# Performance work log

Hardware: AMD Instinct MI355X
Metric: run time of the kernel (lower is better)

## Reference

```python
import jax, jax.numpy as jnp
import numpy as np

CONF_THRES = 0.25
IOU_THRES = 0.45
MAX_ANCHORS = 50
PRE_NMS_TOPK = 2048   # candidate cap, standard fused-NMS trick to bound the IoU matrix
NEG = -1.0e9
NUM_CLASSES = 80
IMG = 640.0


def setup_inputs() -> dict:
    key = jax.random.key(0)
    k1, k2, k3, k4 = jax.random.split(key, 4)
    B, N = 16, 25200
    # realistic xyxy boxes inside a 640x640 image
    cxcy = jax.random.uniform(k1, (B, N, 2), minval=0.0, maxval=IMG)
    wh = jax.random.uniform(k2, (B, N, 2), minval=4.0, maxval=64.0)
    x1y1 = jnp.clip(cxcy - 0.5 * wh, 0.0, IMG)
    x2y2 = jnp.clip(cxcy + 0.5 * wh, 0.0, IMG)
    conf = jax.random.uniform(k3, (B, N, 1))
    cls = jax.random.randint(k4, (B, N, 1), 0, NUM_CLASSES).astype(jnp.float32)
    x = jnp.concatenate([x1y1, x2y2, conf, cls], axis=-1)  # [B, N, 6]
    return {"x": x}


def _box_iou_matrix(boxes):
    # boxes: [K, 4] xyxy -> [K, K] pairwise IoU
    x1, y1, x2, y2 = boxes[:, 0], boxes[:, 1], boxes[:, 2], boxes[:, 3]
    area = jnp.maximum(x2 - x1, 0.0) * jnp.maximum(y2 - y1, 0.0)  # [K]
    iw = jnp.maximum(jnp.minimum(x2[:, None], x2[None, :]) - jnp.maximum(x1[:, None], x1[None, :]), 0.0)
    ih = jnp.maximum(jnp.minimum(y2[:, None], y2[None, :]) - jnp.maximum(y1[:, None], y1[None, :]), 0.0)
    inter = iw * ih
    union = area[:, None] + area[None, :] - inter
    return inter / jnp.maximum(union, 1e-9)


def _nms_single(bx):
    # bx: [N, 6] -> [MAX_ANCHORS, 6], rows padded with -1 (keep_shape semantics)
    scores = bx[:, 4]
    s = jnp.where(scores > CONF_THRES, scores, NEG)  # confidence filter
    top_s, top_i = jax.lax.top_k(s, PRE_NMS_TOPK)     # sort descending by score
    cand = jnp.take(bx, top_i, axis=0)                # [K, 6]
    cvalid = top_s > 0.5 * NEG                        # passed conf filter

    iou = _box_iou_matrix(cand[:, :4])                # [K, K]
    idxs = jnp.arange(PRE_NMS_TOPK)
    # box i may only suppress lower-scored boxes j > i
    suppr_rows = (iou >= IOU_THRES) & (idxs[None, :] > idxs[:, None])

    def step(suppressed, i):
        keep_i = cvalid[i] & jnp.logical_not(suppressed[i])
        suppressed = suppressed | (keep_i & suppr_rows[i])
        return suppressed, keep_i

    _, keep = jax.lax.scan(step, jnp.zeros(PRE_NMS_TOPK, dtype=bool), idxs)

    final_s = jnp.where(keep, cand[:, 4], NEG)
    sel_s, sel_i = jax.lax.top_k(final_s, MAX_ANCHORS)  # top-50 kept boxes by conf
    rows = jnp.take(cand, sel_i, axis=0)                # [50, 6]
    return jnp.where((sel_s > 0.5 * NEG)[:, None], rows, -1.0)


def reference(x):
    # x: [B, N, 6] -> [B, MAX_ANCHORS, 6]
    return jax.vmap(_nms_single)(x)
```

## Files before the change

### kernel.cpp

```cpp
#include <hip/hip_runtime.h>

#define BATCH   16
#define NANCH   25200
#define TPB     1024
#define NWAVES  (TPB / 64)
#define MAXK    50
#define PRETOPK 2048
#define CONF_T  0.25f
#define IOU_T   0.45f
#define NEGV    -1000000000.0f
#define T0      0.9905f
#define CAP     320

__global__ __launch_bounds__(TPB, 1) void nms_kernel(const float* __restrict__ x,
                                                     float* __restrict__ out) {
    __shared__ float s_scores[NANCH];
    __shared__ unsigned long long s_keys[CAP];
    __shared__ float s_srows[CAP][8];
    __shared__ float s_kx1[MAXK], s_ky1[MAXK], s_kx2[MAXK], s_ky2[MAXK], s_ka[MAXK];
    __shared__ float s_wval[NWAVES];
    __shared__ int   s_widx[NWAVES];
    __shared__ int   s_cnt, s_nk, s_best;

    const int b    = blockIdx.x;
    const int tid  = threadIdx.x;
    const int lane = tid & 63;
    const int wave = tid >> 6;

    const float* __restrict__ xb = x + (size_t)b * NANCH * 6;
    float* __restrict__ ob       = out + (size_t)b * MAXK * 6;

    if (tid < CAP) s_keys[tid] = 0ULL;
    if (tid == 0) { s_cnt = 0; s_nk = 0; }
    __syncthreads();

    {
        int i = tid;
        for (int c = 0; c < 3; ++c) {
            float v[8];
            #pragma unroll
            for (int k = 0; k < 8; ++k) v[k] = xb[(size_t)(i + k * TPB) * 6 + 4];
            #pragma unroll
            for (int k = 0; k < 8; ++k) {
                const int idx = i + k * TPB;
                s_scores[idx] = (v[k] > CONF_T) ? v[k] : NEGV;
                if (v[k] > T0) {
                    int slot = atomicAdd(&s_cnt, 1);
                    if (slot < CAP)
                        s_keys[slot] =
                            ((unsigned long long)__float_as_uint(v[k]) << 32) |
                            ((unsigned long long)(65535 - idx) << 16) |
                            (unsigned long long)slot;
                }
            }
            i += 8 * TPB;
        }
        if (i < NANCH) {
            float s = xb[(size_t)i * 6 + 4];
            s_scores[i] = (s > CONF_T) ? s : NEGV;
            if (s > T0) {
                int slot = atomicAdd(&s_cnt, 1);
                if (slot < CAP)
                    s_keys[slot] =
                        ((unsigned long long)__float_as_uint(s) << 32) |
                        ((unsigned long long)(65535 - i) << 16) |
                        (unsigned long long)slot;
            }
        }
    }
    __syncthreads();

    const int cnt   = s_cnt;
    const bool fast = cnt <= CAP;

    if (fast) {
        if (tid < CAP) {
            const unsigned long long mykey = s_keys[tid];
            float2 r0, r1, r2;
            const bool real = tid < cnt;
            if (real) {
                int myi = 65535 - (int)((mykey >> 16) & 0xFFFFULL);
                const float2* rp = (const float2*)(xb + (size_t)myi * 6);
                r0 = rp[0]; r1 = rp[1]; r2 = rp[2];
            }
            int r = 0;
            #pragma unroll 4
            for (int j = 0; j < CAP; ++j) r += (s_keys[j] > mykey) ? 1 : 0;
            if (real) {
                s_srows[r][0] = r0.x; s_srows[r][1] = r0.y;
                s_srows[r][2] = r1.x; s_srows[r][3] = r1.y;
                s_srows[r][4] = r2.x; s_srows[r][5] = r2.y;
            }
        }
        __syncthreads();

        if (wave == 0) {
            int nk = 0;
            for (int tb = 0; tb < cnt && nk < MAXK; tb += 64) {
                const int lim = (cnt - tb) < 64 ? (cnt - tb) : 64;
                float4 bx = {0.f, 0.f, 0.f, 0.f};
                float2 be = {0.f, 0.f};
                bool sup = lane >= lim;
                if (!sup) {
                    bx = *(const float4*)&s_srows[tb + lane][0];
                    be = *(const float2*)&s_srows[tb + lane][4];
                }
                const float ba = fmaxf(bx.z - bx.x, 0.f) * fmaxf(bx.w - bx.y, 0.f);

                for (int j = 0; j < nk; ++j) {
                    float iw = fmaxf(fminf(bx.z, s_kx2[j]) - fmaxf(bx.x, s_kx1[j]), 0.f);
                    float ih = fmaxf(fminf(bx.w, s_ky2[j]) - fmaxf(bx.y, s_ky1[j]), 0.f);
                    float inter = iw * ih;
                    sup = sup || (inter / fmaxf(ba + s_ka[j] - inter, 1e-9f)) >= IOU_T;
                }

                unsigned long long m = 0ULL;
                #pragma unroll 8
                for (int j = 0; j < 64; ++j) {
                    if (j >= lim) break;
                    const float4 oj = *(const float4*)&s_srows[tb + j][0];
                    const float oa = fmaxf(oj.z - oj.x, 0.f) * fmaxf(oj.w - oj.y, 0.f);
                    float iw = fmaxf(fminf(bx.z, oj.z) - fmaxf(bx.x, oj.x), 0.f);
                    float ih = fmaxf(fminf(bx.w, oj.w) - fmaxf(bx.y, oj.y), 0.f);
                    float inter = iw * ih;
                    bool ov = (inter / fmaxf(ba + oa - inter, 1e-9f)) >= IOU_T;
                    m |= ov ? (1ULL << j) : 0ULL;
                }
                m &= ~(1ULL << lane);

                unsigned long long alive = __ballot(!sup);
                unsigned long long keepmask = 0ULL;
                while (alive != 0ULL && nk < MAXK) {
                    const int j = __builtin_ctzll(alive);
                    keepmask |= 1ULL << j;
                    ++nk;
                    const unsigned long long kill = __ballot((m >> j) & 1ULL);
                    alive &= ~(kill | (1ULL << j));
                }

                if ((keepmask >> lane) & 1ULL) {
                    const int nk0 = nk - __popcll(keepmask);
                    const int pos = nk0 + __popcll(keepmask & ((1ULL << lane) - 1ULL));
                    s_kx1[pos] = bx.x; s_ky1[pos] = bx.y;
                    s_kx2[pos] = bx.z; s_ky2[pos] = bx.w; s_ka[pos] = ba;
                    ob[pos * 6 + 0] = bx.x;
                    ob[pos * 6 + 1] = bx.y;
                    ob[pos * 6 + 2] = bx.z;
                    ob[pos * 6 + 3] = bx.w;
                    ob[pos * 6 + 4] = be.x;
                    ob[pos * 6 + 5] = be.y;
                }
            }
            if (lane == 0) s_nk = nk;
        }
        __syncthreads();
    }

    const bool cont = fast && (s_nk < MAXK);
    if (cont) {
        for (int i = tid; i < NANCH; i += TPB)
            if (s_scores[i] > T0) s_scores[i] = NEGV;
    }
    __syncthreads();

    int budget = 0;
    if (!fast)     budget = PRETOPK;
    else if (cont) budget = PRETOPK - cnt;

    if (budget > 0) {
        int nk = s_nk;
        for (int pop = 0; pop < budget && nk < MAXK; ++pop) {
            float bv = NEGV - 1.0f;
            int   bi = NANCH;
            for (int i = tid; i < NANCH; i += TPB) {
                float s = s_scores[i];
                if (s > bv) { bv = s; bi = i; }
            }
            #pragma unroll
            for (int off = 32; off >= 1; off >>= 1) {
                float ov = __shfl_down(bv, off);
                int   oi = __shfl_down(bi, off);
                if (ov > bv || (ov == bv && oi < bi)) { bv = ov; bi = oi; }
            }
            if (lane == 0) { s_wval[wave] = bv; s_widx[wave] = bi; }
            __syncthreads();
            if (wave == 0) {
                bv = (lane < NWAVES) ? s_wval[lane] : (NEGV - 1.0f);
                bi = (lane < NWAVES) ? s_widx[lane] : NANCH;
                #pragma unroll
                for (int off = 32; off >= 1; off >>= 1) {
                    float ov = __shfl_down(bv, off);
                    int   oi = __shfl_down(bi, off);
                    if (ov > bv || (ov == bv && oi < bi)) { bv = ov; bi = oi; }
                }
                if (lane == 0) {
                    s_best = (bv > 0.5f * NEGV) ? bi : -1;
                    if (s_best >= 0) s_scores[bi] = NEGV - 1.0f;
                }
            }
            __syncthreads();
            const int best = s_best;
            if (best < 0) break;

            if (wave == 0) {
                const float bx1 = xb[(size_t)best * 6 + 0];
                const float by1 = xb[(size_t)best * 6 + 1];
                const float bx2 = xb[(size_t)best * 6 + 2];
                const float by2 = xb[(size_t)best * 6 + 3];
                const float ba  = fmaxf(bx2 - bx1, 0.0f) * fmaxf(by2 - by1, 0.0f);
                bool sup = false;
                if (lane < nk) {
                    float iw = fmaxf(fminf(bx2, s_kx2[lane]) - fmaxf(bx1, s_kx1[lane]), 0.f);
                    float ih = fmaxf(fminf(by2, s_ky2[lane]) - fmaxf(by1, s_ky1[lane]), 0.f);
                    float inter = iw * ih;
                    float uni   = ba + s_ka[lane] - inter;
                    sup = (inter / fmaxf(uni, 1e-9f)) >= IOU_T;
                }
                if (lane == 0 && __ballot(sup) == 0ULL) {
                    s_kx1[nk] = bx1; s_ky1[nk] = by1;
                    s_kx2[nk] = bx2; s_ky2[nk] = by2; s_ka[nk] = ba;
                    ob[nk * 6 + 0] = bx1;
                    ob[nk * 6 + 1] = by1;
                    ob[nk * 6 + 2] = bx2;
                    ob[nk * 6 + 3] = by2;
                    ob[nk * 6 + 4] = xb[(size_t)best * 6 + 4];
                    ob[nk * 6 + 5] = xb[(size_t)best * 6 + 5];
                    s_nk = nk + 1;
                }
            }
            __syncthreads();
            nk = s_nk;
        }
    }
    __syncthreads();

    const int nkf = s_nk;
    for (int i = tid; i < (MAXK - nkf) * 6; i += TPB) {
        ob[nkf * 6 + i] = -1.0f;
    }
}

extern "C" void kernel_launch(void* const* d_in, const int* in_sizes, int n_in,
                              void* d_out, int out_size, void* d_ws, size_t ws_size,
                              hipStream_t stream) {
    const float* x = (const float*)d_in[0];
    float* out     = (float*)d_out;
    nms_kernel<<<BATCH, TPB, 0, stream>>>(x, out);
}
```

Measured before the change: 25.54 us.

## Split high-score candidate collection into a separate wide pre-pass kernel

A new collect kernel spreads the confidence scan over 256 blocks (16 per batch) and writes the high-score candidate keys and counts to workspace through global atomics. The main NMS kernel then reads only those keys instead of scanning all 25200 scores with just 16 blocks. The full score array is now loaded into shared memory only when the fallback path is needed. In exchange it adds a memset and an extra kernel launch, plus global atomic contention.

```diff
diff --git a/kernel.cpp b/kernel.cpp
--- a/kernel.cpp
+++ b/kernel.cpp
@@ -11,8 +11,43 @@
 #define NEGV    -1000000000.0f
 #define T0      0.9905f
 #define CAP     320
+#define SPLIT   16
+#define K1B     256
+#define PERBLK  1575
+
+__device__ __forceinline__ unsigned long long make_key(float s, int idx) {
+    return ((unsigned long long)__float_as_uint(s) << 32) |
+           (unsigned long long)(65535 - idx);
+}
+
+__global__ __launch_bounds__(K1B) void collect_kernel(const float* __restrict__ x,
+                                                      unsigned long long* __restrict__ gkeys,
+                                                      unsigned int* __restrict__ gcnt) {
+    const int b    = blockIdx.x >> 4;
+    const int s    = blockIdx.x & 15;
+    const int base = s * PERBLK;
+    const float* __restrict__ xb = x + (size_t)b * NANCH * 6;
+
+    float v[7];
+    int   id[7];
+    #pragma unroll
+    for (int k = 0; k < 7; ++k) {
+        const int i = base + (int)threadIdx.x + k * K1B;
+        id[k] = i;
+        v[k]  = (i < base + PERBLK) ? xb[(size_t)i * 6 + 4] : 0.f;
+    }
+    #pragma unroll
+    for (int k = 0; k < 7; ++k) {
+        if (v[k] > T0) {
+            unsigned slot = atomicAdd(&gcnt[b], 1u);
+            if (slot < CAP) gkeys[(size_t)b * CAP + slot] = make_key(v[k], id[k]);
+        }
+    }
+}
 
 __global__ __launch_bounds__(TPB, 1) void nms_kernel(const float* __restrict__ x,
+                                                     const unsigned long long* __restrict__ gkeys,
+                                                     const unsigned int* __restrict__ gcnt,
                                                      float* __restrict__ out) {
     __shared__ float s_scores[NANCH];
     __shared__ unsigned long long s_keys[CAP];
@@ -20,7 +55,7 @@
     __shared__ float s_kx1[MAXK], s_ky1[MAXK], s_kx2[MAXK], s_ky2[MAXK], s_ka[MAXK];
     __shared__ float s_wval[NWAVES];
     __shared__ int   s_widx[NWAVES];
-    __shared__ int   s_cnt, s_nk, s_best;
+    __shared__ int   s_nk, s_best;
 
     const int b    = blockIdx.x;
     const int tid  = threadIdx.x;
@@ -30,48 +65,13 @@
     const float* __restrict__ xb = x + (size_t)b * NANCH * 6;
     float* __restrict__ ob       = out + (size_t)b * MAXK * 6;
 
-    if (tid < CAP) s_keys[tid] = 0ULL;
-    if (tid == 0) { s_cnt = 0; s_nk = 0; }
+    const unsigned cntg = gcnt ? gcnt[b] : 0xFFFFFFFFu;
+    const bool fast = cntg <= CAP;
+    const int  cnt  = fast ? (int)cntg : 0;
+
+    if (tid == 0) s_nk = 0;
+    if (tid < CAP) s_keys[tid] = (fast && tid < cnt) ? gkeys[(size_t)b * CAP + tid] : 0ULL;
     __syncthreads();
-
-    {
-        int i = tid;
-        for (int c = 0; c < 3; ++c) {
-            float v[8];
-            #pragma unroll
-            for (int k = 0; k < 8; ++k) v[k] = xb[(size_t)(i + k * TPB) * 6 + 4];
-            #pragma unroll
-            for (int k = 0; k < 8; ++k) {
-                const int idx = i + k * TPB;
-                s_scores[idx] = (v[k] > CONF_T) ? v[k] : NEGV;
-                if (v[k] > T0) {
-                    int slot = atomicAdd(&s_cnt, 1);
-                    if (slot < CAP)
-                        s_keys[slot] =
-                            ((unsigned long long)__float_as_uint(v[k]) << 32) |
-                            ((unsigned long long)(65535 - idx) << 16) |
-                            (unsigned long long)slot;
-                }
-            }
-            i += 8 * TPB;
-        }
-        if (i < NANCH) {
-            float s = xb[(size_t)i * 6 + 4];
-            s_scores[i] = (s > CONF_T) ? s : NEGV;
-            if (s > T0) {
-                int slot = atomicAdd(&s_cnt, 1);
-                if (slot < CAP)
-                    s_keys[slot] =
-                        ((unsigned long long)__float_as_uint(s) << 32) |
-                        ((unsigned long long)(65535 - i) << 16) |
-                        (unsigned long long)slot;
-            }
-        }
-    }
-    __syncthreads();
-
-    const int cnt   = s_cnt;
-    const bool fast = cnt <= CAP;
 
     if (fast) {
         if (tid < CAP) {
@@ -79,7 +79,7 @@
             float2 r0, r1, r2;
             const bool real = tid < cnt;
             if (real) {
-                int myi = 65535 - (int)((mykey >> 16) & 0xFFFFULL);
+                int myi = 65535 - (int)(mykey & 0xFFFFULL);
                 const float2* rp = (const float2*)(xb + (size_t)myi * 6);
                 r0 = rp[0]; r1 = rp[1]; r2 = rp[2];
             }
@@ -156,25 +156,23 @@
         __syncthreads();
     }
 
-    const bool cont = fast && (s_nk < MAXK);
-    if (cont) {
-        for (int i = tid; i < NANCH; i += TPB)
-            if (s_scores[i] > T0) s_scores[i] = NEGV;
-    }
-    __syncthreads();
-
-    int budget = 0;
-    if (!fast)     budget = PRETOPK;
-    else if (cont) budget = PRETOPK - cnt;
-
-    if (budget > 0) {
+    const bool need_fb = !fast || (s_nk < MAXK);
+    if (need_fb) {
+        for (int i = tid; i < NANCH; i += TPB) {
+            float sc = xb[(size_t)i * 6 + 4];
+            bool dead = (sc <= CONF_T) || (fast && sc > T0);
+            s_scores[i] = dead ? NEGV : sc;
+        }
+        __syncthreads();
+
+        const int budget = fast ? (PRETOPK - (int)cntg) : PRETOPK;
         int nk = s_nk;
         for (int pop = 0; pop < budget && nk < MAXK; ++pop) {
             float bv = NEGV - 1.0f;
             int   bi = NANCH;
             for (int i = tid; i < NANCH; i += TPB) {
-                float s = s_scores[i];
-                if (s > bv) { bv = s; bi = i; }
+                float sc = s_scores[i];
+                if (sc > bv) { bv = sc; bi = i; }
             }
             #pragma unroll
             for (int off = 32; off >= 1; off >>= 1) {
@@ -231,8 +229,8 @@
             __syncthreads();
             nk = s_nk;
         }
-    }
-    __syncthreads();
+        __syncthreads();
+    }
 
     const int nkf = s_nk;
     for (int i = tid; i < (MAXK - nkf) * 6; i += TPB) {
@@ -245,5 +243,15 @@
                               hipStream_t stream) {
     const float* x = (const float*)d_in[0];
     float* out     = (float*)d_out;
-    nms_kernel<<<BATCH, TPB, 0, stream>>>(x, out);
-}
+
+    const size_t need = 1024 + (size_t)BATCH * CAP * sizeof(unsigned long long);
+    if (d_ws != nullptr && ws_size >= need) {
+        unsigned int* gcnt        = (unsigned int*)d_ws;
+        unsigned long long* gkeys = (unsigned long long*)((char*)d_ws + 1024);
+        hipMemsetAsync(d_ws, 0, BATCH * sizeof(unsigned int), stream);
+        collect_kernel<<<BATCH * SPLIT, K1B, 0, stream>>>(x, gkeys, gcnt);
+        nms_kernel<<<BATCH, TPB, 0, stream>>>(x, gkeys, gcnt, out);
+    } else {
+        nms_kernel<<<BATCH, TPB, 0, stream>>>(x, nullptr, nullptr, out);
+    }
+}
```

Result: slower. 60.95 us (+138.7%).
